# Kernel optimization log

Hardware: AMD Instinct MI355X
Metric: run time of the kernel (lower is better)

## Reference

```python
import jax, jax.numpy as jnp
import numpy as np

N_LAYERS = 2
D_MODEL = 1024
EXPAND = 2
D_INNER = EXPAND * D_MODEL   # 2048
D_STATE = 16
D_CONV = 4
DT_RANK = (D_MODEL + 15) // 16  # 64
BATCH = 2
SEQ = 1024


def setup_inputs() -> dict:
    key = jax.random.key(0)
    ks = jax.random.split(key, 8)
    x = jax.random.normal(ks[0], (BATCH, SEQ, D_MODEL), jnp.float32)
    in_proj_w = jax.random.normal(ks[1], (N_LAYERS, 2 * D_INNER, D_MODEL), jnp.float32) * 0.02
    conv_w = jax.random.normal(ks[2], (N_LAYERS, D_INNER, 1, D_CONV), jnp.float32) * 0.2
    conv_b = jnp.zeros((N_LAYERS, D_INNER), jnp.float32)
    x_proj_w = jax.random.normal(ks[3], (N_LAYERS, DT_RANK + 2 * D_STATE, D_INNER), jnp.float32) * 0.02
    dt_proj_w = jax.random.normal(ks[4], (N_LAYERS, D_INNER, DT_RANK), jnp.float32) * 0.1
    # softplus(b) ~ 0.01 -> realistic small dt init
    dt_proj_b = jnp.full((N_LAYERS, D_INNER), float(np.log(np.expm1(0.01))), jnp.float32)
    A_log = jnp.tile(jnp.log(jnp.arange(1, D_STATE + 1, dtype=jnp.float32))[None, None, :], (N_LAYERS, D_INNER, 1))
    D = jnp.ones((N_LAYERS, D_INNER), jnp.float32)
    out_proj_w = jax.random.normal(ks[5], (N_LAYERS, D_MODEL, D_INNER), jnp.float32) * 0.02
    return {
        'x': x, 'in_proj_w': in_proj_w, 'conv_w': conv_w, 'conv_b': conv_b,
        'x_proj_w': x_proj_w, 'dt_proj_w': dt_proj_w, 'dt_proj_b': dt_proj_b,
        'A_log': A_log, 'D': D, 'out_proj_w': out_proj_w,
    }


def _mamba_block(x, W_in, w_c, b_c, W_x, W_dt, b_dt, A_log, Dp, W_out):
    # x: (B, L, d_model)
    xz = jnp.einsum('bld,ed->ble', x, W_in)           # (B, L, 2*d_inner)
    xc, z = jnp.split(xz, 2, axis=-1)
    # causal depthwise conv1d over time
    xc = xc.transpose(0, 2, 1)                         # (B, d_inner, L)
    xc = jax.lax.conv_general_dilated(
        xc, w_c, window_strides=(1,), padding=[(D_CONV - 1, 0)],
        dimension_numbers=('NCH', 'OIH', 'NCH'), feature_group_count=D_INNER,
    ) + b_c[None, :, None]
    u = jax.nn.silu(xc).transpose(0, 2, 1)             # (B, L, d_inner)
    # input-dependent dt, B, C
    x_dbl = jnp.einsum('bld,ed->ble', u, W_x)          # (B, L, dt_rank+2N)
    dt, Bm, Cm = jnp.split(x_dbl, [DT_RANK, DT_RANK + D_STATE], axis=-1)
    delta = jax.nn.softplus(jnp.einsum('blr,dr->bld', dt, W_dt) + b_dt)  # (B, L, d_inner)
    A = -jnp.exp(A_log)                                 # (d_inner, N)
    dA = jnp.exp(jnp.einsum('bld,dn->bldn', delta, A))  # (B, L, d_inner, N)
    dBu = jnp.einsum('bld,bln,bld->bldn', delta, Bm, u) # (B, L, d_inner, N)

    def step(h, inp):
        dA_t, dBu_t, C_t = inp                          # (B,d,N), (B,d,N), (B,N)
        h = dA_t * h + dBu_t
        return h, jnp.einsum('bdn,bn->bd', h, C_t)

    h0 = jnp.zeros((x.shape[0], D_INNER, D_STATE), x.dtype)
    _, ys = jax.lax.scan(step, h0, (dA.transpose(1, 0, 2, 3), dBu.transpose(1, 0, 2, 3), Cm.transpose(1, 0, 2)))
    y = ys.transpose(1, 0, 2) + u * Dp                  # (B, L, d_inner)
    y = y * jax.nn.silu(z)
    return jnp.einsum('bld,od->blo', y, W_out)          # (B, L, d_model)


def _forward(x, in_proj_w, conv_w, conv_b, x_proj_w, dt_proj_w, dt_proj_b, A_log, D, out_proj_w):
    residual = x
    for i in range(N_LAYERS):
        x = _mamba_block(x, in_proj_w[i], conv_w[i], conv_b[i], x_proj_w[i],
                         dt_proj_w[i], dt_proj_b[i], A_log[i], D[i], out_proj_w[i])
    return x + residual


def reference(x, in_proj_w, conv_w, conv_b, x_proj_w, dt_proj_w, dt_proj_b, A_log, D, out_proj_w):
    return _forward(x, in_proj_w, conv_w, conv_b, x_proj_w, dt_proj_w, dt_proj_b, A_log, D, out_proj_w)
```

## Files before the change

kernel.cpp:

```cpp
#include <hip/hip_runtime.h>
#include <hip/hip_bf16.h>

#define NLAYERS 2
#define DMODEL 1024
#define DINNER 2048
#define DSTATE 16
#define DCONV 4
#define DTRANK 64
#define BATCH 2
#define SEQ 1024
#define TOK (BATCH * SEQ)

#define NCHUNK 32
#define CLEN (SEQ / NCHUNK)
#define KSX 16
#define KSO 4

typedef short bf16x8 __attribute__((ext_vector_type(8)));
typedef float f32x4 __attribute__((ext_vector_type(4)));
typedef unsigned short ushort8 __attribute__((ext_vector_type(8)));

__device__ __forceinline__ float softplusf(float x) {
    return (x > 20.f) ? x : log1pf(__expf(x));
}
__device__ __forceinline__ float siluf(float x) {
    return x / (1.f + __expf(-x));
}
__device__ __forceinline__ unsigned short f2bf(float f) {
    union { float f; unsigned int u; } v; v.f = f;
    const unsigned int r = (v.u + 0x7FFFu + ((v.u >> 16) & 1u)) >> 16;
    return (unsigned short)r;
}
__device__ __forceinline__ float bf2f(unsigned short s) {
    union { unsigned int u; float f; } v; v.u = ((unsigned int)s) << 16;
    return v.f;
}

__device__ __forceinline__ void cvt8(const float* __restrict__ in,
                                     unsigned short* __restrict__ out, int i) {
    const float4 a = reinterpret_cast<const float4*>(in)[i * 2 + 0];
    const float4 b = reinterpret_cast<const float4*>(in)[i * 2 + 1];
    ushort4 o0, o1;
    o0.x = f2bf(a.x); o0.y = f2bf(a.y); o0.z = f2bf(a.z); o0.w = f2bf(a.w);
    o1.x = f2bf(b.x); o1.y = f2bf(b.y); o1.z = f2bf(b.z); o1.w = f2bf(b.w);
    reinterpret_cast<ushort4*>(out)[i * 2 + 0] = o0;
    reinterpret_cast<ushort4*>(out)[i * 2 + 1] = o1;
}

#define WI8 1048576
#define WO8 524288
#define WX8 49152
#define WD8 32768
#define AC8 262144
__global__ __launch_bounds__(256)
void cvt_all(const float* __restrict__ wi, const float* __restrict__ wo,
             const float* __restrict__ wx, const float* __restrict__ wd,
             const float* __restrict__ xin,
             unsigned short* __restrict__ wi_bf, unsigned short* __restrict__ wo_bf,
             unsigned short* __restrict__ wx_bf, unsigned short* __restrict__ wd_bf,
             unsigned short* __restrict__ act_bf) {
    int i = blockIdx.x * 256 + threadIdx.x;
    if (i < WI8) { cvt8(wi, wi_bf, i); return; }
    i -= WI8;
    if (i < WO8) { cvt8(wo, wo_bf, i); return; }
    i -= WO8;
    if (i < WX8) { cvt8(wx, wx_bf, i); return; }
    i -= WX8;
    if (i < WD8) { cvt8(wd, wd_bf, i); return; }
    i -= WD8;
    if (i < AC8) { cvt8(xin, act_bf, i); return; }
}

template <int EPI>
__global__ __launch_bounds__(256)
void gemm_bf16(const unsigned short* __restrict__ Ab, int lda,
               const unsigned short* __restrict__ Wb, int ldw,
               void* __restrict__ Cptr, int ldc, int kLen, int Nw,
               size_t cSlice, const float* __restrict__ bias) {
    __shared__ unsigned short As[3][128 * 32];
    __shared__ unsigned short Bs[3][128 * 32];
    const int tid = threadIdx.x;
    const int wave = tid >> 6, lane = tid & 63;
    const int wr = wave >> 1, wc = wave & 1;
    const int m0 = blockIdx.y * 128, n0 = blockIdx.x * 128;
    const int kbeg = blockIdx.z * kLen;
    const int r = lane & 15, kq = lane >> 4;
    const int nt = kLen >> 5;

    const int ch0 = tid, ch1 = 256 + tid;
    const int sm0 = ch0 >> 2, sk0 = (ch0 & 3) * 8;
    const int sm1 = ch1 >> 2, sk1 = (ch1 & 3) * 8;
    const int wrow0 = min(n0 + sm0, Nw - 1);
    const int wrow1 = min(n0 + sm1, Nw - 1);

    auto stage = [&](int buf, int kt) {
        __builtin_amdgcn_global_load_lds(
            (const __attribute__((address_space(1))) void*)
                &Ab[(size_t)(m0 + sm0) * lda + kt + sk0],
            (__attribute__((address_space(3))) void*)&As[buf][ch0 * 8], 16, 0, 0);
        __builtin_amdgcn_global_load_lds(
            (const __attribute__((address_space(1))) void*)
                &Wb[(size_t)wrow0 * ldw + kt + sk0],
            (__attribute__((address_space(3))) void*)&Bs[buf][ch0 * 8], 16, 0, 0);
        __builtin_amdgcn_global_load_lds(
            (const __attribute__((address_space(1))) void*)
                &Ab[(size_t)(m0 + sm1) * lda + kt + sk1],
            (__attribute__((address_space(3))) void*)&As[buf][ch1 * 8], 16, 0, 0);
        __builtin_amdgcn_global_load_lds(
            (const __attribute__((address_space(1))) void*)
                &Wb[(size_t)wrow1 * ldw + kt + sk1],
            (__attribute__((address_space(3))) void*)&Bs[buf][ch1 * 8], 16, 0, 0);
    };

    f32x4 acc[4][4] = {};
    stage(0, kbeg);
    if (nt > 1) stage(1, kbeg + 32);
    for (int t = 0; t < nt; ++t) {
        const int cur = t % 3;
        if (t + 2 < nt) {
            stage((t + 2) % 3, kbeg + (t + 2) * 32);
            asm volatile("s_waitcnt vmcnt(8)" ::: "memory");
        } else if (t + 1 < nt) {
            asm volatile("s_waitcnt vmcnt(4)" ::: "memory");
        } else {
            asm volatile("s_waitcnt vmcnt(0)" ::: "memory");
        }
        __builtin_amdgcn_s_barrier();
        __builtin_amdgcn_sched_barrier(0);
        bf16x8 a[4], b[4];
#pragma unroll
        for (int f = 0; f < 4; ++f) {
            a[f] = *reinterpret_cast<const bf16x8*>(
                &As[cur][(wr * 64 + f * 16 + r) * 32 + kq * 8]);
            b[f] = *reinterpret_cast<const bf16x8*>(
                &Bs[cur][(wc * 64 + f * 16 + r) * 32 + kq * 8]);
        }
#pragma unroll
        for (int fi = 0; fi < 4; ++fi)
#pragma unroll
            for (int fj = 0; fj < 4; ++fj)
                acc[fi][fj] = __builtin_amdgcn_mfma_f32_16x16x32_bf16(
                    a[fi], b[fj], acc[fi][fj], 0, 0, 0);
        __builtin_amdgcn_sched_barrier(0);
        asm volatile("s_waitcnt lgkmcnt(0)" ::: "memory");
        __builtin_amdgcn_s_barrier();
    }

    const int cr = lane >> 4, cc = lane & 15;
#pragma unroll
    for (int fi = 0; fi < 4; ++fi)
#pragma unroll
        for (int fj = 0; fj < 4; ++fj)
#pragma unroll
            for (int p = 0; p < 4; ++p) {
                const int m = m0 + wr * 64 + fi * 16 + cr * 4 + p;
                const int n = n0 + wc * 64 + fj * 16 + cc;
                const float v = acc[fi][fj][p];
                if (EPI == 0) {
                    if (n < Nw)
                        ((float*)Cptr)[(size_t)blockIdx.z * cSlice +
                                       (size_t)m * ldc + n] = v;
                } else if (EPI == 3) {
                    ((unsigned short*)Cptr)[(size_t)blockIdx.z * cSlice +
                                            (size_t)m * ldc + n] = f2bf(v);
                } else if (EPI == 4) {
                    ((unsigned short*)Cptr)[(size_t)m * ldc + n] =
                        f2bf(softplusf(v + bias[n]));
                } else {
                    if (n < Nw)
                        ((unsigned short*)Cptr)[(size_t)blockIdx.z * cSlice +
                                                (size_t)m * ldc + n] = f2bf(v);
                }
            }
}

__global__ __launch_bounds__(256)
void conv_silu8(const unsigned short* __restrict__ xz_bf,
                const float* __restrict__ cw,
                const float* __restrict__ cb,
                unsigned short* __restrict__ u_bf) {
    const int gid = blockIdx.x * 256 + threadIdx.x;
    const int d8 = gid & 255;
    const int t = gid >> 8;
    const int l = t & (SEQ - 1);
    const int d0 = d8 * 8;

    float cwv[8][4];
#pragma unroll
    for (int j = 0; j < 8; ++j) {
        const float4 c = *reinterpret_cast<const float4*>(&cw[(d0 + j) * DCONV]);
        cwv[j][0] = c.x; cwv[j][1] = c.y; cwv[j][2] = c.z; cwv[j][3] = c.w;
    }
    float acc[8];
    {
        const float4 b0 = *reinterpret_cast<const float4*>(&cb[d0]);
        const float4 b1 = *reinterpret_cast<const float4*>(&cb[d0 + 4]);
        acc[0] = b0.x; acc[1] = b0.y; acc[2] = b0.z; acc[3] = b0.w;
        acc[4] = b1.x; acc[5] = b1.y; acc[6] = b1.z; acc[7] = b1.w;
    }
#pragma unroll
    for (int k = 0; k < DCONV; ++k) {
        const int li = l - (DCONV - 1) + k;
        if (li >= 0) {
            const ushort8 v = *reinterpret_cast<const ushort8*>(
                &xz_bf[(size_t)(t - (DCONV - 1) + k) * 4096 + d0]);
#pragma unroll
            for (int j = 0; j < 8; ++j)
                acc[j] = fmaf(cwv[j][k], bf2f(v[j]), acc[j]);
        }
    }
    ushort8 o;
#pragma unroll
    for (int j = 0; j < 8; ++j) o[j] = f2bf(siluf(acc[j]));
    *reinterpret_cast<ushort8*>(&u_bf[(size_t)t * DINNER + d0]) = o;
}

__global__ __launch_bounds__(256)
void reduce_x(const unsigned short* __restrict__ part, float* __restrict__ xdbl,
              unsigned short* __restrict__ dt_bf) {
    const int i = blockIdx.x * 256 + threadIdx.x;
    if (i >= TOK * 96) return;
    float s = 0.f;
#pragma unroll
    for (int k = 0; k < KSX; ++k) s += bf2f(part[(size_t)k * (TOK * 96) + i]);
    xdbl[i] = s;
    const int t = i / 96, c = i - t * 96;
    if (c < DTRANK) dt_bf[t * DTRANK + c] = f2bf(s);
}

template <int MODE>
__global__ __launch_bounds__(256)
void reduce_out(const unsigned short* __restrict__ part,
                const float* __restrict__ resid, void* __restrict__ outp) {
    const int i = blockIdx.x * 256 + threadIdx.x;
    if (i >= TOK * DMODEL / 4) return;
    float s[4] = {0.f, 0.f, 0.f, 0.f};
#pragma unroll
    for (int k = 0; k < KSO; ++k) {
        const ushort4 p = reinterpret_cast<const ushort4*>(
            &part[(size_t)k * (TOK * DMODEL)])[i];
        s[0] += bf2f(p.x); s[1] += bf2f(p.y); s[2] += bf2f(p.z); s[3] += bf2f(p.w);
    }
    if (MODE == 0) {
        ushort4 o;
        o.x = f2bf(s[0]); o.y = f2bf(s[1]); o.z = f2bf(s[2]); o.w = f2bf(s[3]);
        reinterpret_cast<ushort4*>(outp)[i] = o;
    } else {
        const float4 rr = reinterpret_cast<const float4*>(resid)[i];
        float4 o;
        o.x = s[0] + rr.x; o.y = s[1] + rr.y; o.z = s[2] + rr.z; o.w = s[3] + rr.w;
        reinterpret_cast<float4*>(outp)[i] = o;
    }
}

__device__ __forceinline__ void load_b16(const float* __restrict__ p, float* B) {
    const float4* bp = reinterpret_cast<const float4*>(p);
    const float4 b0 = bp[0], b1 = bp[1], b2 = bp[2], b3 = bp[3];
    B[0] = b0.x; B[1] = b0.y; B[2] = b0.z; B[3] = b0.w;
    B[4] = b1.x; B[5] = b1.y; B[6] = b1.z; B[7] = b1.w;
    B[8] = b2.x; B[9] = b2.y; B[10] = b2.z; B[11] = b2.w;
    B[12] = b3.x; B[13] = b3.y; B[14] = b3.z; B[15] = b3.w;
}
__device__ __forceinline__ void load_bf16x16(const unsigned short* __restrict__ p,
                                             float* B) {
    const ushort8 v0 = *reinterpret_cast<const ushort8*>(p);
    const ushort8 v1 = *reinterpret_cast<const ushort8*>(p + 8);
#pragma unroll
    for (int j = 0; j < 8; ++j) { B[j] = bf2f(v0[j]); B[8 + j] = bf2f(v1[j]); }
}
__device__ __forceinline__ void store_bf16x16(unsigned short* __restrict__ p,
                                              const float* B) {
    ushort8 v0, v1;
#pragma unroll
    for (int j = 0; j < 8; ++j) { v0[j] = f2bf(B[j]); v1[j] = f2bf(B[8 + j]); }
    *reinterpret_cast<ushort8*>(p) = v0;
    *reinterpret_cast<ushort8*>(p + 8) = v1;
}

__global__ __launch_bounds__(256)
void scan_partial(const unsigned short* __restrict__ delta_bf,
                  const unsigned short* __restrict__ u_bf,
                  const float* __restrict__ xdbl,
                  const float* __restrict__ A_log,
                  unsigned short* __restrict__ hbuf,
                  unsigned short* __restrict__ Pbuf) {
    const int b = blockIdx.y / NCHUNK;
    const int c = blockIdx.y % NCHUNK;
    const int d = blockIdx.x * 256 + threadIdx.x;
    const int t0 = b * SEQ + c * CLEN;

    float A_dn[16];
    load_b16(&A_log[d * DSTATE], A_dn);
#pragma unroll
    for (int n = 0; n < 16; ++n) A_dn[n] = -__expf(A_dn[n]);

    float h[16];
#pragma unroll
    for (int n = 0; n < 16; ++n) h[n] = 0.f;
    float sdlt = 0.f;

    float dltA, uvA, BA[16];
    float dltB, uvB, BB[16];
    dltA = bf2f(delta_bf[(size_t)t0 * DINNER + d]);
    uvA = bf2f(u_bf[(size_t)t0 * DINNER + d]);
    load_b16(&xdbl[(size_t)t0 * 96 + DTRANK], BA);

#define PSTEP(dlt_, uv_, Bc_)                              \
    {                                                      \
        const float du = (dlt_) * (uv_);                   \
        sdlt += (dlt_);                                    \
        _Pragma("unroll")                                  \
        for (int n = 0; n < 16; ++n) {                     \
            const float dA = __expf((dlt_) * A_dn[n]);     \
            h[n] = fmaf(dA, h[n], du * Bc_[n]);            \
        }                                                  \
    }

    for (int l = 0; l < CLEN; l += 2) {
        const int t = t0 + l;
        dltB = bf2f(delta_bf[(size_t)(t + 1) * DINNER + d]);
        uvB = bf2f(u_bf[(size_t)(t + 1) * DINNER + d]);
        load_b16(&xdbl[(size_t)(t + 1) * 96 + DTRANK], BB);
        PSTEP(dltA, uvA, BA);
        if (l + 2 < CLEN) {
            dltA = bf2f(delta_bf[(size_t)(t + 2) * DINNER + d]);
            uvA = bf2f(u_bf[(size_t)(t + 2) * DINNER + d]);
            load_b16(&xdbl[(size_t)(t + 2) * 96 + DTRANK], BA);
        }
        PSTEP(dltB, uvB, BB);
    }
#undef PSTEP

    float P[16];
#pragma unroll
    for (int n = 0; n < 16; ++n) P[n] = __expf(sdlt * A_dn[n]);

    const size_t base = ((size_t)(b * NCHUNK + c) * DINNER + d) * DSTATE;
    store_bf16x16(&hbuf[base], h);
    store_bf16x16(&Pbuf[base], P);
}

__global__ __launch_bounds__(256)
void scan_combine(unsigned short* __restrict__ hbuf,
                  const unsigned short* __restrict__ Pbuf) {
    const int gid = blockIdx.x * 256 + threadIdx.x;
    const int b = gid / (DINNER * DSTATE);
    const int dn = gid - b * (DINNER * DSTATE);
    const size_t base = (size_t)b * NCHUNK * DINNER * DSTATE + dn;
    float hv[NCHUNK], Pv[NCHUNK];
#pragma unroll
    for (int c = 0; c < NCHUNK; ++c) {
        const size_t idx = base + (size_t)c * (DINNER * DSTATE);
        hv[c] = bf2f(hbuf[idx]);
        Pv[c] = bf2f(Pbuf[idx]);
    }
    float hi = 0.f;
#pragma unroll
    for (int c = 0; c < NCHUNK; ++c) {
        const size_t idx = base + (size_t)c * (DINNER * DSTATE);
        hbuf[idx] = f2bf(hi);
        hi = fmaf(Pv[c], hi, hv[c]);
    }
}

__global__ __launch_bounds__(256)
void scan_final(const unsigned short* __restrict__ delta_bf,
                const unsigned short* __restrict__ u_bf,
                const float* __restrict__ xdbl,
                const unsigned short* __restrict__ xz_bf,
                const float* __restrict__ A_log,
                const float* __restrict__ Dp,
                const unsigned short* __restrict__ hbuf,
                unsigned short* __restrict__ yout) {
    const int b = blockIdx.y / NCHUNK;
    const int c = blockIdx.y % NCHUNK;
    const int d = blockIdx.x * 256 + threadIdx.x;
    const int t0 = b * SEQ + c * CLEN;

    float A_dn[16];
    load_b16(&A_log[d * DSTATE], A_dn);
#pragma unroll
    for (int n = 0; n < 16; ++n) A_dn[n] = -__expf(A_dn[n]);
    const float Dd = Dp[d];

    float h[16];
    load_bf16x16(&hbuf[((size_t)(b * NCHUNK + c) * DINNER + d) * DSTATE], h);

    float dltA, uvA, BA[16], CA[16];
    float dltB, uvB, BB[16], CB[16];
    dltA = bf2f(delta_bf[(size_t)t0 * DINNER + d]);
    uvA = bf2f(u_bf[(size_t)t0 * DINNER + d]);
    load_b16(&xdbl[(size_t)t0 * 96 + DTRANK], BA);
    load_b16(&xdbl[(size_t)t0 * 96 + DTRANK + DSTATE], CA);

#define FSTEP(t_, dlt_, uv_, Bc_, Cc_)                          \
    {                                                           \
        const float du = (dlt_) * (uv_);                        \
        _Pragma("unroll")                                       \
        for (int n = 0; n < 16; ++n) {                          \
            const float dA = __expf((dlt_) * A_dn[n]);          \
            h[n] = fmaf(dA, h[n], du * Bc_[n]);                 \
        }                                                       \
        float s0 = 0.f, s1 = 0.f, s2 = 0.f, s3 = 0.f;           \
        _Pragma("unroll")                                       \
        for (int q = 0; q < 4; ++q) {                           \
            s0 = fmaf(h[q*4+0], Cc_[q*4+0], s0);                \
            s1 = fmaf(h[q*4+1], Cc_[q*4+1], s1);                \
            s2 = fmaf(h[q*4+2], Cc_[q*4+2], s2);                \
            s3 = fmaf(h[q*4+3], Cc_[q*4+3], s3);                \
        }                                                       \
        const float zv = bf2f(xz_bf[(size_t)(t_) * 4096 + 2048 + d]); \
        const float y = (s0 + s1) + (s2 + s3) + (uv_) * Dd;     \
        yout[(size_t)(t_) * DINNER + d] = f2bf(y * siluf(zv));  \
    }

    for (int l = 0; l < CLEN; l += 2) {
        const int t = t0 + l;
        dltB = bf2f(delta_bf[(size_t)(t + 1) * DINNER + d]);
        uvB = bf2f(u_bf[(size_t)(t + 1) * DINNER + d]);
        load_b16(&xdbl[(size_t)(t + 1) * 96 + DTRANK], BB);
        load_b16(&xdbl[(size_t)(t + 1) * 96 + DTRANK + DSTATE], CB);
        FSTEP(t, dltA, uvA, BA, CA);
        if (l + 2 < CLEN) {
            dltA = bf2f(delta_bf[(size_t)(t + 2) * DINNER + d]);
            uvA = bf2f(u_bf[(size_t)(t + 2) * DINNER + d]);
            load_b16(&xdbl[(size_t)(t + 2) * 96 + DTRANK], BA);
            load_b16(&xdbl[(size_t)(t + 2) * 96 + DTRANK + DSTATE], CA);
        }
        FSTEP(t + 1, dltB, uvB, BB, CB);
    }
#undef FSTEP
}

extern "C" void kernel_launch(void* const* d_in, const int* in_sizes, int n_in,
                              void* d_out, int out_size, void* d_ws, size_t ws_size,
                              hipStream_t stream) {
    const float* x          = (const float*)d_in[0];
    const float* in_proj_w  = (const float*)d_in[1];
    const float* conv_w     = (const float*)d_in[2];
    const float* conv_b     = (const float*)d_in[3];
    const float* x_proj_w   = (const float*)d_in[4];
    const float* dt_proj_w  = (const float*)d_in[5];
    const float* dt_proj_b  = (const float*)d_in[6];
    const float* A_log      = (const float*)d_in[7];
    const float* Dp         = (const float*)d_in[8];
    const float* out_proj_w = (const float*)d_in[9];
    float* out = (float*)d_out;

    float* ws = (float*)d_ws;
    float* xdbl  = ws;
    unsigned short* us = (unsigned short*)(xdbl + 196608);
    unsigned short* xpart  = us;
    unsigned short* hbuf   = xpart + 3145728;
    unsigned short* Pbuf   = hbuf + 2097152;
    unsigned short* opart  = Pbuf + 2097152;
    unsigned short* wi_bf  = opart + 8388608;
    unsigned short* wo_bf  = wi_bf + 8388608;
    unsigned short* wx_bf  = wo_bf + 4194304;
    unsigned short* wd_bf  = wx_bf + 393216;
    unsigned short* xz_bf  = wd_bf + 262144;
    unsigned short* u_bf   = xz_bf + 8388608;
    unsigned short* dlt_bf = u_bf  + 4194304;
    unsigned short* act_bf = dlt_bf + 4194304;
    unsigned short* y_bf   = act_bf + 2097152;
    unsigned short* dt_bf  = y_bf  + 4194304;

    cvt_all<<<(WI8 + WO8 + WX8 + WD8 + AC8 + 255) / 256, 256, 0, stream>>>(
        in_proj_w, out_proj_w, x_proj_w, dt_proj_w, x,
        wi_bf, wo_bf, wx_bf, wd_bf, act_bf);

    for (int layer = 0; layer < NLAYERS; ++layer) {
        const unsigned short* Wi = wi_bf + (size_t)layer * (2 * DINNER) * DMODEL;
        const unsigned short* Wo = wo_bf + (size_t)layer * DMODEL * DINNER;
        const unsigned short* Wx = wx_bf + (size_t)layer * 96 * DINNER;
        const unsigned short* Wd = wd_bf + (size_t)layer * DINNER * DTRANK;
        const float* cw = conv_w    + (size_t)layer * DINNER * DCONV;
        const float* cb = conv_b    + (size_t)layer * DINNER;
        const float* bd = dt_proj_b + (size_t)layer * DINNER;
        const float* Al = A_log     + (size_t)layer * DINNER * DSTATE;
        const float* Dl = Dp        + (size_t)layer * DINNER;

        {
            dim3 grid(4096 / 128, TOK / 128, 1);
            gemm_bf16<3><<<grid, 256, 0, stream>>>(act_bf, DMODEL, Wi, DMODEL,
                                                   xz_bf, 2 * DINNER, DMODEL,
                                                   2 * DINNER, 0, nullptr);
        }
        conv_silu8<<<(TOK * 256) / 256, 256, 0, stream>>>(xz_bf, cw, cb, u_bf);
        {
            dim3 grid(1, TOK / 128, KSX);
            gemm_bf16<5><<<grid, 256, 0, stream>>>(u_bf, DINNER, Wx, DINNER,
                                                   xpart, 96, DINNER / KSX, 96,
                                                   (size_t)TOK * 96, nullptr);
            reduce_x<<<(TOK * 96 + 255) / 256, 256, 0, stream>>>(xpart, xdbl, dt_bf);
        }
        {
            dim3 grid(DINNER / 128, TOK / 128, 1);
            gemm_bf16<4><<<grid, 256, 0, stream>>>(dt_bf, DTRANK, Wd, DTRANK,
                                                   dlt_bf, DINNER, DTRANK, DINNER,
                                                   0, bd);
        }
        {
            dim3 gridA(DINNER / 256, BATCH * NCHUNK);
            scan_partial<<<gridA, 256, 0, stream>>>(dlt_bf, u_bf, xdbl, Al,
                                                    hbuf, Pbuf);
            scan_combine<<<(BATCH * DINNER * DSTATE) / 256, 256, 0, stream>>>(hbuf, Pbuf);
            scan_final<<<gridA, 256, 0, stream>>>(dlt_bf, u_bf, xdbl, xz_bf,
                                                  Al, Dl, hbuf, y_bf);
        }
        {
            dim3 grid(DMODEL / 128, TOK / 128, KSO);
            gemm_bf16<3><<<grid, 256, 0, stream>>>(y_bf, DINNER, Wo, DINNER,
                                                   opart, DMODEL, DINNER / KSO,
                                                   DMODEL, (size_t)TOK * DMODEL,
                                                   nullptr);
            const int nred = TOK * DMODEL / 4;
            if (layer == NLAYERS - 1) {
                reduce_out<1><<<(nred + 255) / 256, 256, 0, stream>>>(opart, x, out);
            } else {
                reduce_out<0><<<(nred + 255) / 256, 256, 0, stream>>>(opart, nullptr,
                                                                      act_bf);
            }
        }
    }
}
```

Before: 324.4 us.

## Swizzle GEMM LDS layout and shrink to double-buffered pipeline

```diff
diff --git a/kernel.cpp b/kernel.cpp
--- a/kernel.cpp
+++ b/kernel.cpp
@@ -34,6 +34,10 @@
 __device__ __forceinline__ float bf2f(unsigned short s) {
     union { unsigned int u; float f; } v; v.u = ((unsigned int)s) << 16;
     return v.f;
+}
+
+__device__ __forceinline__ int swz_granule(int row, int kq) {
+    return (row >> 1) * 8 + ((((row & 1) << 2) | kq) ^ ((row >> 1) & 7));
 }
 
 __device__ __forceinline__ void cvt8(const float* __restrict__ in,
@@ -77,8 +81,8 @@
                const unsigned short* __restrict__ Wb, int ldw,
                void* __restrict__ Cptr, int ldc, int kLen, int Nw,
                size_t cSlice, const float* __restrict__ bias) {
-    __shared__ unsigned short As[3][128 * 32];
-    __shared__ unsigned short Bs[3][128 * 32];
+    __shared__ unsigned short As[2][128 * 32];
+    __shared__ unsigned short Bs[2][128 * 32];
     const int tid = threadIdx.x;
     const int wave = tid >> 6, lane = tid & 63;
     const int wr = wave >> 1, wc = wave & 1;
@@ -88,39 +92,45 @@
     const int nt = kLen >> 5;
 
     const int ch0 = tid, ch1 = 256 + tid;
-    const int sm0 = ch0 >> 2, sk0 = (ch0 & 3) * 8;
-    const int sm1 = ch1 >> 2, sk1 = (ch1 & 3) * 8;
-    const int wrow0 = min(n0 + sm0, Nw - 1);
-    const int wrow1 = min(n0 + sm1, Nw - 1);
+    const int g0 = ch0 >> 3, p0 = ch0 & 7, lp0 = p0 ^ (g0 & 7);
+    const int srow0 = (g0 << 1) | (lp0 >> 2), skq0 = lp0 & 3;
+    const int g1 = ch1 >> 3, p1 = ch1 & 7, lp1 = p1 ^ (g1 & 7);
+    const int srow1 = (g1 << 1) | (lp1 >> 2), skq1 = lp1 & 3;
+    const int wrow0 = min(n0 + srow0, Nw - 1);
+    const int wrow1 = min(n0 + srow1, Nw - 1);
 
     auto stage = [&](int buf, int kt) {
         __builtin_amdgcn_global_load_lds(
             (const __attribute__((address_space(1))) void*)
-                &Ab[(size_t)(m0 + sm0) * lda + kt + sk0],
+                &Ab[(size_t)(m0 + srow0) * lda + kt + skq0 * 8],
             (__attribute__((address_space(3))) void*)&As[buf][ch0 * 8], 16, 0, 0);
         __builtin_amdgcn_global_load_lds(
             (const __attribute__((address_space(1))) void*)
-                &Wb[(size_t)wrow0 * ldw + kt + sk0],
+                &Wb[(size_t)wrow0 * ldw + kt + skq0 * 8],
             (__attribute__((address_space(3))) void*)&Bs[buf][ch0 * 8], 16, 0, 0);
         __builtin_amdgcn_global_load_lds(
             (const __attribute__((address_space(1))) void*)
-                &Ab[(size_t)(m0 + sm1) * lda + kt + sk1],
+                &Ab[(size_t)(m0 + srow1) * lda + kt + skq1 * 8],
             (__attribute__((address_space(3))) void*)&As[buf][ch1 * 8], 16, 0, 0);
         __builtin_amdgcn_global_load_lds(
             (const __attribute__((address_space(1))) void*)
-                &Wb[(size_t)wrow1 * ldw + kt + sk1],
+                &Wb[(size_t)wrow1 * ldw + kt + skq1 * 8],
             (__attribute__((address_space(3))) void*)&Bs[buf][ch1 * 8], 16, 0, 0);
     };
 
+    int aoff[4], boff[4];
+#pragma unroll
+    for (int f = 0; f < 4; ++f) {
+        aoff[f] = swz_granule(wr * 64 + f * 16 + r, kq) * 8;
+        boff[f] = swz_granule(wc * 64 + f * 16 + r, kq) * 8;
+    }
+
     f32x4 acc[4][4] = {};
     stage(0, kbeg);
-    if (nt > 1) stage(1, kbeg + 32);
     for (int t = 0; t < nt; ++t) {
-        const int cur = t % 3;
-        if (t + 2 < nt) {
-            stage((t + 2) % 3, kbeg + (t + 2) * 32);
-            asm volatile("s_waitcnt vmcnt(8)" ::: "memory");
-        } else if (t + 1 < nt) {
+        const int cur = t & 1;
+        if (t + 1 < nt) {
+            stage(cur ^ 1, kbeg + (t + 1) * 32);
             asm volatile("s_waitcnt vmcnt(4)" ::: "memory");
         } else {
             asm volatile("s_waitcnt vmcnt(0)" ::: "memory");
@@ -130,10 +140,8 @@
         bf16x8 a[4], b[4];
 #pragma unroll
         for (int f = 0; f < 4; ++f) {
-            a[f] = *reinterpret_cast<const bf16x8*>(
-                &As[cur][(wr * 64 + f * 16 + r) * 32 + kq * 8]);
-            b[f] = *reinterpret_cast<const bf16x8*>(
-                &Bs[cur][(wc * 64 + f * 16 + r) * 32 + kq * 8]);
+            a[f] = *reinterpret_cast<const bf16x8*>(&As[cur][aoff[f]]);
+            b[f] = *reinterpret_cast<const bf16x8*>(&Bs[cur][boff[f]]);
         }
 #pragma unroll
         for (int fi = 0; fi < 4; ++fi)
```

After: 320.5 us, median of 2. About the same (-1.2%).
